# Optimization experiments

Hardware: AMD Instinct MI355X
Metric: run time of the kernel (lower is better)

The kernel has to match this reference:

```python
import jax, jax.numpy as jnp
import numpy as np

B = 4096
INPUT = 1024
HIDDEN = 2048
D_INNER = 2 * HIDDEN      # expand=2
DT_RANK = HIDDEN // 16    # 128
D_STATE = 16
LN_EPS = 1e-5


def setup_inputs() -> dict:
    key = jax.random.key(0)
    ks = jax.random.split(key, 12)
    s = lambda fan_in: 1.0 / np.sqrt(fan_in)
    inp = {
        "x": jax.random.normal(ks[0], (B, INPUT), jnp.float32),
        "h": jax.random.normal(ks[1], (B, HIDDEN), jnp.float32),
        # in_proj: Linear(input_size, 2*d_inner, bias=False)
        "W_in": jax.random.uniform(ks[2], (2 * D_INNER, INPUT), jnp.float32, -s(INPUT), s(INPUT)),
        # state_proj: Linear(hidden, d_inner, bias=False)
        "W_state": jax.random.uniform(ks[3], (D_INNER, HIDDEN), jnp.float32, -s(HIDDEN), s(HIDDEN)),
        # x_proj: Linear(d_inner, dt_rank + 2*d_state, bias=False)
        "W_xproj": jax.random.uniform(ks[4], (DT_RANK + 2 * D_STATE, D_INNER), jnp.float32, -s(D_INNER), s(D_INNER)),
        # dt_proj: Linear(dt_rank, d_inner, bias=True), weight ~ U(-dt_rank^-0.5, dt_rank^-0.5)
        "W_dt": jax.random.uniform(ks[5], (D_INNER, DT_RANK), jnp.float32, -s(DT_RANK), s(DT_RANK)),
        "b_dt": jnp.log(jnp.expm1(jnp.exp(jax.random.uniform(ks[6], (D_INNER,), jnp.float32)
                                           * (np.log(0.1) - np.log(0.001)) + np.log(0.001)))),
        # A_log = log(arange(1, d_state+1)) repeated over d_inner (unused in single-step math)
        "A_log": jnp.broadcast_to(jnp.log(jnp.arange(1, D_STATE + 1, dtype=jnp.float32)), (D_INNER, D_STATE)),
        "D": jnp.ones((D_INNER,), jnp.float32),
        # out_proj: Linear(d_inner, hidden, bias=False)
        "W_out": jax.random.uniform(ks[7], (HIDDEN, D_INNER), jnp.float32, -s(D_INNER), s(D_INNER)),
        # LayerNorm(hidden)
        "gamma": jnp.ones((HIDDEN,), jnp.float32),
        "beta": jnp.zeros((HIDDEN,), jnp.float32),
    }
    return inp


def _layernorm(x, gamma, beta):
    mu = jnp.mean(x, axis=-1, keepdims=True)
    var = jnp.mean(jnp.square(x - mu), axis=-1, keepdims=True)
    return (x - mu) * jax.lax.rsqrt(var + LN_EPS) * gamma + beta


def reference(x, h, W_in, W_state, W_xproj, W_dt, b_dt, A_log, D, W_out, gamma, beta):
    # in_proj and split into x branch / gate z
    xz = x @ W_in.T                               # [B, 2*d_inner]
    x_br, z = jnp.split(xz, 2, axis=-1)
    # add projected previous hidden state, then SiLU
    x_br = jax.nn.silu(x_br + h @ W_state.T)      # [B, d_inner]
    # x_proj -> (dt, B_mat, C)
    x_dbl = x_br @ W_xproj.T                      # [B, dt_rank + 2*d_state]
    dt_lo = x_dbl[:, :DT_RANK]
    B_mat = x_dbl[:, DT_RANK:DT_RANK + D_STATE]   # [B, d_state]
    C_mat = x_dbl[:, DT_RANK + D_STATE:]          # [B, d_state]
    dt = jax.nn.softplus(dt_lo @ W_dt.T + b_dt)   # [B, d_inner]
    # ssm_out[b,d] = sum_n dt[b,d]*B[b,n]*x_br[b,d]*C[b,n] + D[d]*x_br[b,d]
    bc = jnp.sum(B_mat * C_mat, axis=-1, keepdims=True)  # [B, 1]
    ssm_out = dt * x_br * bc + D * x_br           # [B, d_inner]
    # gate, output projection, residual, layernorm
    y = ssm_out * jax.nn.silu(z)
    h_new = y @ W_out.T + h
    return _layernorm(h_new, gamma, beta)
```

## Files before the change

kernel.cpp:

```cpp
#include <hip/hip_runtime.h>
#include <hip/hip_bf16.h>
#include <cstdint>
#include <cstddef>

typedef unsigned short u16;
typedef __bf16 bf16x8 __attribute__((ext_vector_type(8)));
typedef float f32x4 __attribute__((ext_vector_type(4)));

#define B_ROWS 4096
#define N_HIDDEN 2048
#define DT_RANK 128

static __device__ __forceinline__ u16 f2bf(float f) {
  unsigned u = __float_as_uint(f);
  u += 0x7FFFu + ((u >> 16) & 1u);
  return (u16)(u >> 16);
}
static __device__ __forceinline__ float bf2f(u16 b) {
  return __uint_as_float(((unsigned)b) << 16);
}
static __device__ __forceinline__ float siluf(float v) {
  return v / (1.0f + __expf(-v));
}
static __device__ __forceinline__ float softplusf(float v) {
  return v > 15.0f ? v : log1pf(__expf(v));
}
static __device__ __forceinline__ void async16(void* lds, const void* g) {
  __builtin_amdgcn_global_load_lds((const __attribute__((address_space(1))) void*)g,
                                   (__attribute__((address_space(3))) void*)lds, 16, 0, 0);
}

struct CvtJobs {
  const float* src[8];
  u16* dst[8];
  int rl4[8];
  int dstride[8];
  int cum[9];
};
__global__ __launch_bounds__(256)
void cvt_all_kernel(CvtJobs J) {
  int b = blockIdx.x;
  int job = 0;
#pragma unroll
  for (int k = 1; k < 8; ++k) if (b >= J.cum[k]) job = k;
  const int row = b - J.cum[job];
  const int rl4 = J.rl4[job];
  const float4* s = (const float4*)(J.src[job] + (size_t)row * (rl4 * 4));
  ushort4* d = (ushort4*)(J.dst[job] + (size_t)row * J.dstride[job]);
  for (int c = threadIdx.x; c < rl4; c += blockDim.x) {
    float4 f = s[c];
    ushort4 o;
    o.x = f2bf(f.x); o.y = f2bf(f.y); o.z = f2bf(f.z); o.w = f2bf(f.w);
    d[c] = o;
  }
}

template <int NN, int KK, int LDA, int LDB, int EPI>
__global__ __launch_bounds__(512, 1)
void gemm8(const u16* __restrict__ A, const u16* __restrict__ Bw,
           float* __restrict__ outf, u16* __restrict__ outb, long long zstride)
{
  extern __shared__ u16 lds[];
  u16* ldsA = lds;
  u16* ldsB = lds + 32768;
  constexpr int NT = KK / 64;
  static_assert(NT >= 2, "schedule assumes NT >= 2");

  const int t = threadIdx.x;
  const int lane = t & 63, w = t >> 6;
  const int wr = w >> 2, wc = w & 3;
  const int r = lane & 15;
  const int q4 = lane >> 4;

  const int gx = gridDim.x;
  const int nwg = gx * gridDim.y;
  const int bid = blockIdx.y * gx + blockIdx.x;
  const int cpx = nwg >> 3;
  const int swz = (bid & 7) * cpx + (bid >> 3);
  const int n0 = (swz % gx) * 256;
  const int m0 = (swz / gx) * 256;
  const int koff = blockIdx.z * KK;

  f32x4 acc[2][2][4][2] = {};

  auto stA = [&](int buf, int half, int k0) {
#pragma unroll
    for (int i = 0; i < 2; ++i) {
      const int ii = w * 2 + i;
      const int c = ii * 64 + lane;
      const int row = c >> 3;
      const int ch = (c & 7) ^ (row & 7);
      async16(ldsA + (buf * 2 + half) * 8192 + ii * 512,
              A + (size_t)(m0 + half * 128 + row) * LDA + (koff + k0 + ch * 8));
    }
  };
  auto stB = [&](int buf, int half, int k0) {
#pragma unroll
    for (int i = 0; i < 2; ++i) {
      const int ii = w * 2 + i;
      const int c = ii * 64 + lane;
      const int row = c >> 3;
      const int ch = (c & 7) ^ (row & 7);
      async16(ldsB + (buf * 2 + half) * 8192 + ii * 512,
              Bw + (size_t)(n0 + half * 128 + row) * LDB + (koff + k0 + ch * 8));
    }
  };

  auto ldA = [&](int buf, int half, int lr, int kki) -> bf16x8 {
    const int tt = kki * 4 + q4;
    return *(const bf16x8*)(ldsA + (size_t)((buf * 2 + half) * 8192 + lr * 64 + ((tt ^ (lr & 7)) << 3)));
  };
  auto ldB = [&](int buf, int half, int lr, int kki) -> bf16x8 {
    const int tt = kki * 4 + q4;
    return *(const bf16x8*)(ldsB + (size_t)((buf * 2 + half) * 8192 + lr * 64 + ((tt ^ (lr & 7)) << 3)));
  };

  stA(0, 0, 0); stB(0, 0, 0); stB(0, 1, 0); stA(0, 1, 0);
  asm volatile("s_waitcnt vmcnt(4)" ::: "memory");
  __builtin_amdgcn_s_barrier();
  asm volatile("" ::: "memory");

  int cur = 0;
  for (int j = 0; j < NT; ++j) {
    const int nxt = cur ^ 1;
    const bool lastj = (j == NT - 1);
    bf16x8 fa[8], fah[8], fb0[4], fb1[4];

#pragma unroll
    for (int fi = 0; fi < 4; ++fi)
#pragma unroll
      for (int ks = 0; ks < 2; ++ks)
        fa[fi * 2 + ks] = ldA(cur, 0, wr * 64 + fi * 16 + r, ks);
#pragma unroll
    for (int g = 0; g < 2; ++g)
#pragma unroll
      for (int ks = 0; ks < 2; ++ks)
        fb0[g * 2 + ks] = ldB(cur, 0, wc * 32 + g * 16 + r, ks);
    if (j + 1 < NT) stA(nxt, 0, (j + 1) * 64);
    asm volatile("" ::: "memory");
    __builtin_amdgcn_s_barrier();
    asm volatile("s_waitcnt lgkmcnt(0)" ::: "memory");
    __builtin_amdgcn_s_setprio(1);
#pragma unroll
    for (int fi = 0; fi < 4; ++fi)
#pragma unroll
      for (int g = 0; g < 2; ++g) {
        acc[0][0][fi][g] = __builtin_amdgcn_mfma_f32_16x16x32_bf16(fa[fi * 2 + 0], fb0[g * 2 + 0], acc[0][0][fi][g], 0, 0, 0);
        acc[0][0][fi][g] = __builtin_amdgcn_mfma_f32_16x16x32_bf16(fa[fi * 2 + 1], fb0[g * 2 + 1], acc[0][0][fi][g], 0, 0, 0);
      }
    __builtin_amdgcn_s_setprio(0);
    if (lastj) { asm volatile("s_waitcnt vmcnt(2)" ::: "memory"); }
    else       { asm volatile("s_waitcnt vmcnt(4)" ::: "memory"); }
    __builtin_amdgcn_s_barrier();
    asm volatile("" ::: "memory");

#pragma unroll
    for (int g = 0; g < 2; ++g)
#pragma unroll
      for (int ks = 0; ks < 2; ++ks)
        fb1[g * 2 + ks] = ldB(cur, 1, wc * 32 + g * 16 + r, ks);
    if (j + 1 < NT) stB(nxt, 0, (j + 1) * 64);
    asm volatile("" ::: "memory");
    __builtin_amdgcn_s_barrier();
    asm volatile("s_waitcnt lgkmcnt(0)" ::: "memory");
    __builtin_amdgcn_s_setprio(1);
#pragma unroll
    for (int fi = 0; fi < 4; ++fi)
#pragma unroll
      for (int g = 0; g < 2; ++g) {
        acc[0][1][fi][g] = __builtin_amdgcn_mfma_f32_16x16x32_bf16(fa[fi * 2 + 0], fb1[g * 2 + 0], acc[0][1][fi][g], 0, 0, 0);
        acc[0][1][fi][g] = __builtin_amdgcn_mfma_f32_16x16x32_bf16(fa[fi * 2 + 1], fb1[g * 2 + 1], acc[0][1][fi][g], 0, 0, 0);
      }
    __builtin_amdgcn_s_setprio(0);
    if (lastj) { asm volatile("s_waitcnt vmcnt(0)" ::: "memory"); }
    else       { asm volatile("s_waitcnt vmcnt(4)" ::: "memory"); }
    __builtin_amdgcn_s_barrier();
    asm volatile("" ::: "memory");

#pragma unroll
    for (int fi = 0; fi < 4; ++fi)
#pragma unroll
      for (int ks = 0; ks < 2; ++ks)
        fah[fi * 2 + ks] = ldA(cur, 1, wr * 64 + fi * 16 + r, ks);
    if (j + 1 < NT) stB(nxt, 1, (j + 1) * 64);
    asm volatile("" ::: "memory");
    __builtin_amdgcn_s_barrier();
    asm volatile("s_waitcnt lgkmcnt(0)" ::: "memory");
    __builtin_amdgcn_s_setprio(1);
#pragma unroll
    for (int fi = 0; fi < 4; ++fi)
#pragma unroll
      for (int g = 0; g < 2; ++g) {
        acc[1][0][fi][g] = __builtin_amdgcn_mfma_f32_16x16x32_bf16(fah[fi * 2 + 0], fb0[g * 2 + 0], acc[1][0][fi][g], 0, 0, 0);
        acc[1][0][fi][g] = __builtin_amdgcn_mfma_f32_16x16x32_bf16(fah[fi * 2 + 1], fb0[g * 2 + 1], acc[1][0][fi][g], 0, 0, 0);
      }
    __builtin_amdgcn_s_setprio(0);
    asm volatile("" ::: "memory");
    __builtin_amdgcn_s_barrier();
    asm volatile("" ::: "memory");

    if (j + 1 < NT) stA(nxt, 1, (j + 1) * 64);
    asm volatile("" ::: "memory");
    __builtin_amdgcn_s_barrier();
    __builtin_amdgcn_s_setprio(1);
#pragma unroll
    for (int fi = 0; fi < 4; ++fi)
#pragma unroll
      for (int g = 0; g < 2; ++g) {
        acc[1][1][fi][g] = __builtin_amdgcn_mfma_f32_16x16x32_bf16(fah[fi * 2 + 0], fb1[g * 2 + 0], acc[1][1][fi][g], 0, 0, 0);
        acc[1][1][fi][g] = __builtin_amdgcn_mfma_f32_16x16x32_bf16(fah[fi * 2 + 1], fb1[g * 2 + 1], acc[1][1][fi][g], 0, 0, 0);
      }
    __builtin_amdgcn_s_setprio(0);
    if (j + 1 < NT) { asm volatile("s_waitcnt vmcnt(4)" ::: "memory"); }
    asm volatile("" ::: "memory");
    __builtin_amdgcn_s_barrier();
    asm volatile("" ::: "memory");
    cur = nxt;
  }

  float* of = outf ? (outf + (size_t)blockIdx.z * zstride) : nullptr;
#pragma unroll
  for (int a = 0; a < 2; ++a)
#pragma unroll
    for (int b = 0; b < 2; ++b)
#pragma unroll
      for (int fi = 0; fi < 4; ++fi)
#pragma unroll
        for (int g = 0; g < 2; ++g)
#pragma unroll
          for (int tt = 0; tt < 4; ++tt) {
            const int grow = m0 + a * 128 + wr * 64 + fi * 16 + q4 * 4 + tt;
            const int gcol = n0 + b * 128 + wc * 32 + g * 16 + r;
            const float v = acc[a][b][fi][g][tt];
            if constexpr (EPI == 0) {
              outb[(size_t)grow * NN + gcol] = f2bf(siluf(v));
            } else {
              of[(size_t)grow * NN + gcol] = v;
            }
          }
}

template <int NN, int KK, int LDA, int EPI>
__global__ __launch_bounds__(256)
void gemm_bt(const u16* __restrict__ A, const u16* __restrict__ Bw,
             float* __restrict__ outf, u16* __restrict__ outb,
             const float* __restrict__ aux1, const float* __restrict__ aux2,
             const float* __restrict__ aux3,
             const u16* __restrict__ xaux, const u16* __restrict__ saux)
{
  constexpr int BM = 128, BK = 64;
  __shared__ alignas(16) u16 As[2][BM * BK];
  __shared__ alignas(16) u16 Bs[2][BM * BK];
  const int t = threadIdx.x;
  const int lane = t & 63, w = t >> 6;
  const int m0 = blockIdx.y * BM, n0 = blockIdx.x * BM;
  const int mw = (w >> 1) * 64, nw = (w & 1) * 64;
  const int r = lane & 15;
  const int kq = (lane >> 4) * 8;

  f32x4 acc[4][4] = {};

  auto stage = [&](int buf, int k0) {
#pragma unroll
    for (int i = 0; i < 4; ++i) {
      const int slot0 = (w * 4 + i) * 64;
      const int s = slot0 + lane;
      const int row = s >> 3, cs = (s & 7) * 8;
      async16(&As[buf][slot0 * 8], A + (size_t)(m0 + row) * LDA + k0 + cs);
      async16(&Bs[buf][slot0 * 8], Bw + (size_t)(n0 + row) * KK + k0 + cs);
    }
  };

  stage(0, 0);
  asm volatile("s_waitcnt vmcnt(0)" ::: "memory");
  __syncthreads();
  int cur = 0;

  for (int k0 = 0; k0 < KK; k0 += BK) {
    if (k0 + BK < KK) stage(cur ^ 1, k0 + BK);
#pragma unroll
    for (int kk = 0; kk < BK; kk += 32) {
      bf16x8 af[4], bb[4];
#pragma unroll
      for (int f = 0; f < 4; ++f)
        af[f] = *(const bf16x8*)(&As[cur][(mw + f * 16 + r) * BK + kk + kq]);
#pragma unroll
      for (int f = 0; f < 4; ++f)
        bb[f] = *(const bf16x8*)(&Bs[cur][(nw + f * 16 + r) * BK + kk + kq]);
#pragma unroll
      for (int fm = 0; fm < 4; ++fm)
#pragma unroll
        for (int fn = 0; fn < 4; ++fn)
          acc[fm][fn] = __builtin_amdgcn_mfma_f32_16x16x32_bf16(af[fm], bb[fn], acc[fm][fn], 0, 0, 0);
    }
    asm volatile("s_waitcnt vmcnt(0)" ::: "memory");
    __syncthreads();
    cur ^= 1;
  }

  const int rr = (lane >> 4) * 4;
  const int cc = lane & 15;
#pragma unroll
  for (int fm = 0; fm < 4; ++fm) {
#pragma unroll
    for (int fn = 0; fn < 4; ++fn) {
#pragma unroll
      for (int tt = 0; tt < 4; ++tt) {
        const int grow = m0 + mw + fm * 16 + rr + tt;
        const int gcol = n0 + nw + fn * 16 + cc;
        float v = acc[fm][fn][tt];
        if constexpr (EPI == 2) {
          float dt = softplusf(v + aux1[gcol]);
          float xv = bf2f(xaux[(size_t)grow * NN + gcol]);
          float sv = bf2f(saux[(size_t)grow * NN + gcol]);
          float yv = xv * (dt * aux2[grow] + aux3[gcol]) * sv;
          outb[(size_t)grow * NN + gcol] = f2bf(yv);
        } else {
          outf[(size_t)grow * NN + gcol] = v;
        }
      }
    }
  }
}

__global__ __launch_bounds__(256)
void gemm_xproj(const u16* __restrict__ A, const u16* __restrict__ Bw,
                float* __restrict__ part)
{
  constexpr int BK = 64;
  __shared__ alignas(16) u16 As[64 * BK];
  __shared__ alignas(16) u16 Bs[160 * BK];
  const int t = threadIdx.x, lane = t & 63, w = t >> 6;
  const int m0 = blockIdx.x * 64;
  const int kz = blockIdx.y;
  const int r = lane & 15, kq = (lane >> 4) * 8;
  f32x4 acc[10] = {};
  for (int kt = 0; kt < 1024; kt += BK) {
    const int k0 = kz * 1024 + kt;
#pragma unroll
    for (int i = 0; i < 2; ++i) {
      const int slot0 = (w * 2 + i) * 64;
      const int s = slot0 + lane;
      async16(As + slot0 * 8, A + (size_t)(m0 + (s >> 3)) * 4096 + k0 + (s & 7) * 8);
    }
#pragma unroll
    for (int i = 0; i < 5; ++i) {
      const int slot0 = (w * 5 + i) * 64;
      const int s = slot0 + lane;
      async16(Bs + slot0 * 8, Bw + (size_t)(s >> 3) * 4096 + k0 + (s & 7) * 8);
    }
    asm volatile("s_waitcnt vmcnt(0)" ::: "memory");
    __syncthreads();
#pragma unroll
    for (int kk = 0; kk < BK; kk += 32) {
      bf16x8 af = *(const bf16x8*)(As + (w * 16 + r) * BK + kk + kq);
#pragma unroll
      for (int fn = 0; fn < 10; ++fn) {
        bf16x8 bb = *(const bf16x8*)(Bs + (fn * 16 + r) * BK + kk + kq);
        acc[fn] = __builtin_amdgcn_mfma_f32_16x16x32_bf16(af, bb, acc[fn], 0, 0, 0);
      }
    }
    __syncthreads();
  }
  float* o = part + (size_t)kz * B_ROWS * 160;
  const int rr = (lane >> 4) * 4, cc = lane & 15;
#pragma unroll
  for (int fn = 0; fn < 10; ++fn)
#pragma unroll
    for (int tt = 0; tt < 4; ++tt)
      o[(size_t)(m0 + w * 16 + rr + tt) * 160 + fn * 16 + cc] = acc[fn][tt];
}

__global__ __launch_bounds__(192)
void xdbl_reduce(const float* __restrict__ part, u16* __restrict__ dtlo,
                 float* __restrict__ bc)
{
  const int row = blockIdx.x, t = threadIdx.x;
  __shared__ float cvals[32];
  float v = 0.0f;
  if (t < 160) {
    const float* p = part + (size_t)row * 160 + t;
#pragma unroll
    for (int z = 0; z < 4; ++z) v += p[(size_t)z * B_ROWS * 160];
  }
  if (t < DT_RANK) dtlo[(size_t)row * DT_RANK + t] = f2bf(v);
  if (t >= DT_RANK && t < 160) cvals[t - DT_RANK] = v;
  __syncthreads();
  if (t == 0) {
    float s = 0.0f;
#pragma unroll
    for (int j = 0; j < 16; ++j) s += cvals[j] * cvals[j + 16];
    bc[row] = s;
  }
}

__global__ __launch_bounds__(256)
void ln_kernel(const float* __restrict__ p0, const float* __restrict__ p1,
               const float* __restrict__ hh, const float* __restrict__ gamma,
               const float* __restrict__ beta, float* __restrict__ out)
{
  const int row = blockIdx.x, t = threadIdx.x;
  __shared__ float red[4];
  const float4* x0 = (const float4*)(p0 + (size_t)row * N_HIDDEN);
  const float4* x1 = (const float4*)(p1 + (size_t)row * N_HIDDEN);
  const float4* xh = (const float4*)(hh + (size_t)row * N_HIDDEN);
  float4 a, b;
  {
    float4 u = x0[t], v = x1[t], w = xh[t];
    a.x = u.x + v.x + w.x; a.y = u.y + v.y + w.y; a.z = u.z + v.z + w.z; a.w = u.w + v.w + w.w;
    u = x0[t + 256]; v = x1[t + 256]; w = xh[t + 256];
    b.x = u.x + v.x + w.x; b.y = u.y + v.y + w.y; b.z = u.z + v.z + w.z; b.w = u.w + v.w + w.w;
  }
  float s = ((a.x + a.y) + (a.z + a.w)) + ((b.x + b.y) + (b.z + b.w));
#pragma unroll
  for (int m = 32; m; m >>= 1) s += __shfl_xor(s, m);
  if ((t & 63) == 0) red[t >> 6] = s;
  __syncthreads();
  s = (red[0] + red[1]) + (red[2] + red[3]);
  const float mu = s * (1.0f / N_HIDDEN);
  float dx0 = a.x - mu, dx1 = a.y - mu, dx2 = a.z - mu, dx3 = a.w - mu;
  float dy0 = b.x - mu, dy1 = b.y - mu, dy2 = b.z - mu, dy3 = b.w - mu;
  float q = ((dx0 * dx0 + dx1 * dx1) + (dx2 * dx2 + dx3 * dx3)) +
            ((dy0 * dy0 + dy1 * dy1) + (dy2 * dy2 + dy3 * dy3));
  __syncthreads();
#pragma unroll
  for (int m = 32; m; m >>= 1) q += __shfl_xor(q, m);
  if ((t & 63) == 0) red[t >> 6] = q;
  __syncthreads();
  q = (red[0] + red[1]) + (red[2] + red[3]);
  const float inv = rsqrtf(q * (1.0f / N_HIDDEN) + 1e-5f);
  const float4 ga = ((const float4*)gamma)[t], gb = ((const float4*)gamma)[t + 256];
  const float4 ba = ((const float4*)beta)[t], bbv = ((const float4*)beta)[t + 256];
  float4 o0, o1;
  o0.x = dx0 * inv * ga.x + ba.x;
  o0.y = dx1 * inv * ga.y + ba.y;
  o0.z = dx2 * inv * ga.z + ba.z;
  o0.w = dx3 * inv * ga.w + ba.w;
  o1.x = dy0 * inv * gb.x + bbv.x;
  o1.y = dy1 * inv * gb.y + bbv.y;
  o1.z = dy2 * inv * gb.z + bbv.z;
  o1.w = dy3 * inv * gb.w + bbv.w;
  float4* o4 = (float4*)(out + (size_t)row * N_HIDDEN);
  o4[t] = o0;
  o4[t + 256] = o1;
}

extern "C" void kernel_launch(void* const* d_in, const int* in_sizes, int n_in,
                              void* d_out, int out_size, void* d_ws, size_t ws_size,
                              hipStream_t stream) {
  const float* x     = (const float*)d_in[0];
  const float* h     = (const float*)d_in[1];
  const float* W_in  = (const float*)d_in[2];
  const float* W_st  = (const float*)d_in[3];
  const float* W_xp  = (const float*)d_in[4];
  const float* W_dt  = (const float*)d_in[5];
  const float* b_dt  = (const float*)d_in[6];
  const float* Dv    = (const float*)d_in[8];
  const float* W_out = (const float*)d_in[9];
  const float* gamma = (const float*)d_in[10];
  const float* beta  = (const float*)d_in[11];
  float* out = (float*)d_out;
  (void)in_sizes; (void)n_in; (void)out_size; (void)ws_size;

  char* ws = (char*)d_ws;
  size_t o = 0;
  auto alloc = [&](size_t bytes) { char* p = ws + o; o += bytes; return p; };
  u16* Acat    = (u16*)alloc((size_t)4096 * 3072 * 2);
  u16* Wcat    = (u16*)alloc((size_t)4096 * 3072 * 2);
  u16* Wz_bf   = (u16*)alloc((size_t)4096 * 1024 * 2);
  u16* Wxp_bf  = (u16*)alloc((size_t)160 * 4096 * 2);
  u16* Wdt_bf  = (u16*)alloc((size_t)4096 * 128 * 2);
  u16* Wout_bf = (u16*)alloc((size_t)2048 * 4096 * 2);
  u16* xbr_bf  = (u16*)alloc((size_t)4096 * 4096 * 2);
  u16* sz_bf   = (u16*)alloc((size_t)4096 * 4096 * 2);
  float* part  = (float*)alloc((size_t)4 * 4096 * 160 * 4);
  u16* dtlo_bf = (u16*)alloc((size_t)4096 * 128 * 2);
  float* bc    = (float*)alloc((size_t)4096 * 4);
  u16* y_bf = (u16*)Acat;
  float* p0 = (float*)xbr_bf;
  float* p1 = p0 + (size_t)4096 * 2048;

  CvtJobs J;
  J.src[0] = x;                           J.dst[0] = Acat;        J.rl4[0] = 256;  J.dstride[0] = 3072;
  J.src[1] = h;                           J.dst[1] = Acat + 1024; J.rl4[1] = 512;  J.dstride[1] = 3072;
  J.src[2] = W_in;                        J.dst[2] = Wcat;        J.rl4[2] = 256;  J.dstride[2] = 3072;
  J.src[3] = W_st;                        J.dst[3] = Wcat + 1024; J.rl4[3] = 512;  J.dstride[3] = 3072;
  J.src[4] = W_in + (size_t)4096 * 1024;  J.dst[4] = Wz_bf;       J.rl4[4] = 256;  J.dstride[4] = 1024;
  J.src[5] = W_xp;                        J.dst[5] = Wxp_bf;      J.rl4[5] = 1024; J.dstride[5] = 4096;
  J.src[6] = W_dt;                        J.dst[6] = Wdt_bf;      J.rl4[6] = 32;   J.dstride[6] = 128;
  J.src[7] = W_out;                       J.dst[7] = Wout_bf;     J.rl4[7] = 1024; J.dstride[7] = 4096;
  const int rows[8] = {4096, 4096, 4096, 4096, 4096, 160, 4096, 2048};
  J.cum[0] = 0;
  for (int k = 0; k < 8; ++k) J.cum[k + 1] = J.cum[k] + rows[k];
  cvt_all_kernel<<<J.cum[8], 256, 0, stream>>>(J);

  gemm8<4096, 3072, 3072, 3072, 0><<<dim3(16, 16, 1), 512, 131072, stream>>>(
      Acat, Wcat, nullptr, xbr_bf, 0);
  gemm8<4096, 1024, 3072, 1024, 0><<<dim3(16, 16, 1), 512, 131072, stream>>>(
      Acat, Wz_bf, nullptr, sz_bf, 0);
  gemm_xproj<<<dim3(64, 4), 256, 0, stream>>>(xbr_bf, Wxp_bf, part);
  xdbl_reduce<<<4096, 192, 0, stream>>>(part, dtlo_bf, bc);
  gemm_bt<4096, 128, 128, 2><<<dim3(32, 32), 256, 0, stream>>>(
      dtlo_bf, Wdt_bf, nullptr, y_bf, b_dt, bc, Dv, xbr_bf, sz_bf);
  gemm8<2048, 2048, 4096, 4096, 1><<<dim3(8, 16, 2), 512, 131072, stream>>>(
      y_bf, Wout_bf, p0, nullptr, (long long)4096 * 2048);
  ln_kernel<<<4096, 256, 0, stream>>>(p0, p1, h, gamma, beta, out);
}
```

Baseline: 360.4 us.

## Deepen GEMM software pipeline: prefetch next-tile LDS fragments and drop extra barriers

Restructures the gemm8 main loop so that LDS fragment reads for the next k-tile are issued during the current tile's MFMA phases. The A half-tile for two steps ahead is staged into the buffer just freed. Each phase now uses one barrier instead of two, and vmcnt waits are adjusted to the deeper pipeline. This aims to hide LDS read and global load latency behind MFMA work. In exchange it keeps more fragments live in registers, needs NT >= 3, and relies on subtle buffer-reuse ordering that could race.

```diff
diff --git a/kernel.cpp b/kernel.cpp
--- a/kernel.cpp
+++ b/kernel.cpp
@@ -64,7 +64,7 @@
   u16* ldsA = lds;
   u16* ldsB = lds + 32768;
   constexpr int NT = KK / 64;
-  static_assert(NT >= 2, "schedule assumes NT >= 2");
+  static_assert(NT >= 3, "schedule assumes NT >= 3");
 
   const int t = threadIdx.x;
   const int lane = t & 63, w = t >> 6;
@@ -115,31 +115,37 @@
     return *(const bf16x8*)(ldsB + (size_t)((buf * 2 + half) * 8192 + lr * 64 + ((tt ^ (lr & 7)) << 3)));
   };
 
+  bf16x8 fa[8], fah[8], fb0[4], fb1[4];
+
   stA(0, 0, 0); stB(0, 0, 0); stB(0, 1, 0); stA(0, 1, 0);
+  stA(1, 0, 64);
   asm volatile("s_waitcnt vmcnt(4)" ::: "memory");
   __builtin_amdgcn_s_barrier();
   asm volatile("" ::: "memory");
+#pragma unroll
+  for (int fi = 0; fi < 4; ++fi)
+#pragma unroll
+    for (int ks = 0; ks < 2; ++ks)
+      fa[fi * 2 + ks] = ldA(0, 0, wr * 64 + fi * 16 + r, ks);
+#pragma unroll
+  for (int g = 0; g < 2; ++g)
+#pragma unroll
+    for (int ks = 0; ks < 2; ++ks)
+      fb0[g * 2 + ks] = ldB(0, 0, wc * 32 + g * 16 + r, ks);
 
   int cur = 0;
   for (int j = 0; j < NT; ++j) {
     const int nxt = cur ^ 1;
-    const bool lastj = (j == NT - 1);
-    bf16x8 fa[8], fah[8], fb0[4], fb1[4];
-
-#pragma unroll
-    for (int fi = 0; fi < 4; ++fi)
+    const bool t1 = (j + 1 >= NT);
+    const bool t2 = (j + 2 >= NT);
+    const bool deep = (j < NT - 2);
+
+#pragma unroll
+    for (int g = 0; g < 2; ++g)
 #pragma unroll
       for (int ks = 0; ks < 2; ++ks)
-        fa[fi * 2 + ks] = ldA(cur, 0, wr * 64 + fi * 16 + r, ks);
-#pragma unroll
-    for (int g = 0; g < 2; ++g)
-#pragma unroll
-      for (int ks = 0; ks < 2; ++ks)
-        fb0[g * 2 + ks] = ldB(cur, 0, wc * 32 + g * 16 + r, ks);
-    if (j + 1 < NT) stA(nxt, 0, (j + 1) * 64);
-    asm volatile("" ::: "memory");
-    __builtin_amdgcn_s_barrier();
-    asm volatile("s_waitcnt lgkmcnt(0)" ::: "memory");
+        fb1[g * 2 + ks] = ldB(cur, 1, wc * 32 + g * 16 + r, ks);
+    if (!t1) stB(nxt, 0, (j + 1) * 64);
     __builtin_amdgcn_s_setprio(1);
 #pragma unroll
     for (int fi = 0; fi < 4; ++fi)
@@ -149,20 +155,17 @@
         acc[0][0][fi][g] = __builtin_amdgcn_mfma_f32_16x16x32_bf16(fa[fi * 2 + 1], fb0[g * 2 + 1], acc[0][0][fi][g], 0, 0, 0);
       }
     __builtin_amdgcn_s_setprio(0);
-    if (lastj) { asm volatile("s_waitcnt vmcnt(2)" ::: "memory"); }
-    else       { asm volatile("s_waitcnt vmcnt(4)" ::: "memory"); }
+    if (deep) { asm volatile("s_waitcnt vmcnt(4)" ::: "memory"); }
+    else      { asm volatile("s_waitcnt vmcnt(0)" ::: "memory"); }
     __builtin_amdgcn_s_barrier();
     asm volatile("" ::: "memory");
 
 #pragma unroll
-    for (int g = 0; g < 2; ++g)
+    for (int fi = 0; fi < 4; ++fi)
 #pragma unroll
       for (int ks = 0; ks < 2; ++ks)
-        fb1[g * 2 + ks] = ldB(cur, 1, wc * 32 + g * 16 + r, ks);
-    if (j + 1 < NT) stB(nxt, 0, (j + 1) * 64);
-    asm volatile("" ::: "memory");
-    __builtin_amdgcn_s_barrier();
-    asm volatile("s_waitcnt lgkmcnt(0)" ::: "memory");
+        fah[fi * 2 + ks] = ldA(cur, 1, wr * 64 + fi * 16 + r, ks);
+    if (!t1) stB(nxt, 1, (j + 1) * 64);
     __builtin_amdgcn_s_setprio(1);
 #pragma unroll
     for (int fi = 0; fi < 4; ++fi)
@@ -172,20 +175,19 @@
         acc[0][1][fi][g] = __builtin_amdgcn_mfma_f32_16x16x32_bf16(fa[fi * 2 + 1], fb1[g * 2 + 1], acc[0][1][fi][g], 0, 0, 0);
       }
     __builtin_amdgcn_s_setprio(0);
-    if (lastj) { asm volatile("s_waitcnt vmcnt(0)" ::: "memory"); }
-    else       { asm volatile("s_waitcnt vmcnt(4)" ::: "memory"); }
+    if (deep) { asm volatile("s_waitcnt vmcnt(4)" ::: "memory"); }
+    else      { asm volatile("s_waitcnt vmcnt(0)" ::: "memory"); }
     __builtin_amdgcn_s_barrier();
     asm volatile("" ::: "memory");
 
-#pragma unroll
-    for (int fi = 0; fi < 4; ++fi)
-#pragma unroll
-      for (int ks = 0; ks < 2; ++ks)
-        fah[fi * 2 + ks] = ldA(cur, 1, wr * 64 + fi * 16 + r, ks);
-    if (j + 1 < NT) stB(nxt, 1, (j + 1) * 64);
-    asm volatile("" ::: "memory");
-    __builtin_amdgcn_s_barrier();
-    asm volatile("s_waitcnt lgkmcnt(0)" ::: "memory");
+    if (!t1) {
+#pragma unroll
+      for (int fi = 0; fi < 4; ++fi)
+#pragma unroll
+        for (int ks = 0; ks < 2; ++ks)
+          fa[fi * 2 + ks] = ldA(nxt, 0, wr * 64 + fi * 16 + r, ks);
+      stA(nxt, 1, (j + 1) * 64);
+    }
     __builtin_amdgcn_s_setprio(1);
 #pragma unroll
     for (int fi = 0; fi < 4; ++fi)
@@ -195,13 +197,19 @@
         acc[1][0][fi][g] = __builtin_amdgcn_mfma_f32_16x16x32_bf16(fah[fi * 2 + 1], fb0[g * 2 + 1], acc[1][0][fi][g], 0, 0, 0);
       }
     __builtin_amdgcn_s_setprio(0);
-    asm volatile("" ::: "memory");
+    if (deep) { asm volatile("s_waitcnt vmcnt(4)" ::: "memory"); }
+    else      { asm volatile("s_waitcnt vmcnt(0)" ::: "memory"); }
     __builtin_amdgcn_s_barrier();
     asm volatile("" ::: "memory");
 
-    if (j + 1 < NT) stA(nxt, 1, (j + 1) * 64);
-    asm volatile("" ::: "memory");
-    __builtin_amdgcn_s_barrier();
+    if (!t1) {
+#pragma unroll
+      for (int g = 0; g < 2; ++g)
+#pragma unroll
+        for (int ks = 0; ks < 2; ++ks)
+          fb0[g * 2 + ks] = ldB(nxt, 0, wc * 32 + g * 16 + r, ks);
+    }
+    if (!t2) stA(cur, 0, (j + 2) * 64);
     __builtin_amdgcn_s_setprio(1);
 #pragma unroll
     for (int fi = 0; fi < 4; ++fi)
@@ -211,8 +219,8 @@
         acc[1][1][fi][g] = __builtin_amdgcn_mfma_f32_16x16x32_bf16(fah[fi * 2 + 1], fb1[g * 2 + 1], acc[1][1][fi][g], 0, 0, 0);
       }
     __builtin_amdgcn_s_setprio(0);
-    if (j + 1 < NT) { asm volatile("s_waitcnt vmcnt(4)" ::: "memory"); }
-    asm volatile("" ::: "memory");
+    if (deep) { asm volatile("s_waitcnt vmcnt(4)" ::: "memory"); }
+    else      { asm volatile("s_waitcnt vmcnt(0)" ::: "memory"); }
     __builtin_amdgcn_s_barrier();
     asm volatile("" ::: "memory");
     cur = nxt;
```

After: 505.6 us. +40.3%, slower.
